# Optimization experiments

Hardware: AMD Instinct MI355X
Metric: run time of the kernel (lower is better)

Reference implementation:

```python
import jax, jax.numpy as jnp
import numpy as np

N = 50000   # nodes
E = 800000  # edges
H = 128     # hidden dim
V = 50000   # feats_per_node (embedding vocab)


def setup_inputs() -> dict:
    key = jax.random.key(0)
    ks = jax.random.split(key, 16)
    s = 0.05  # keep activations in a sane range
    return {
        "node_ids": jax.random.randint(ks[0], (N,), 0, V),
        "src": jax.random.randint(ks[1], (E,), 0, N),
        "dst": jnp.sort(jax.random.randint(ks[2], (E,), 0, N)),
        "emb": jax.random.normal(ks[3], (V, H), jnp.float32) * s,
        "W_pool1": jax.random.normal(ks[4], (H, H), jnp.float32) * s,
        "b_pool1": jax.random.normal(ks[5], (H,), jnp.float32) * s,
        "W_self1": jax.random.normal(ks[6], (H, H), jnp.float32) * s,
        "W_neigh1": jax.random.normal(ks[7], (H, H), jnp.float32) * s,
        "b1": jax.random.normal(ks[8], (H,), jnp.float32) * s,
        "W_pool2": jax.random.normal(ks[9], (H, H), jnp.float32) * s,
        "b_pool2": jax.random.normal(ks[10], (H,), jnp.float32) * s,
        "W_self2": jax.random.normal(ks[11], (H, H), jnp.float32) * s,
        "W_neigh2": jax.random.normal(ks[12], (H, H), jnp.float32) * s,
        "b2": jax.random.normal(ks[13], (H,), jnp.float32) * s,
    }


def _sage_pool_layer(h, src, dst, W_pool, b_pool, W_self, W_neigh, b):
    # DGL SAGEConv('pool'): per-src MLP, gather over edges, segmented max per dst.
    m = jax.nn.relu(h @ W_pool + b_pool)              # [N, H]
    msgs = m[src]                                     # [E, H] gather
    agg = jax.ops.segment_max(msgs, dst, num_segments=N,
                              indices_are_sorted=True)  # [N, H]
    agg = jnp.where(jnp.isneginf(agg), 0.0, agg)      # zero-in-degree -> 0 (DGL semantics)
    return h @ W_self + agg @ W_neigh + b


def reference(node_ids, src, dst, emb,
              W_pool1, b_pool1, W_self1, W_neigh1, b1,
              W_pool2, b_pool2, W_self2, W_neigh2, b2):
    h = emb[node_ids]                                 # embedding_h on 1-hot indices
    h = _sage_pool_layer(h, src, dst, W_pool1, b_pool1, W_self1, W_neigh1, b1)
    h = _sage_pool_layer(h, src, dst, W_pool2, b_pool2, W_self2, W_neigh2, b2)
    return h
```

## Files before the change

kernel.cpp:

```cpp
#include <hip/hip_runtime.h>

#define HD 128

typedef __attribute__((ext_vector_type(8))) short short8;
typedef __attribute__((ext_vector_type(4))) float floatx4;

typedef unsigned short ushort_t;
typedef unsigned int uint_t;

__device__ __forceinline__ ushort_t f2b(float f) {
    union { float f; uint_t u; } v; v.f = f;
    uint_t r = v.u + 0x7fff + ((v.u >> 16) & 1);
    return (ushort_t)(r >> 16);
}
__device__ __forceinline__ float b_lo(uint_t p) {
    union { uint_t u; float f; } v; v.u = p << 16; return v.f;
}
__device__ __forceinline__ float b_hi(uint_t p) {
    union { uint_t u; float f; } v; v.u = p & 0xffff0000u; return v.f;
}
__device__ __forceinline__ uint_t packb(float a, float b) {
    union { float f; uint_t u; } x, y; x.f = a; y.f = b;
    return (x.u >> 16) | (y.u & 0xffff0000u);
}
__device__ __forceinline__ short8 cvt8(const float* __restrict__ p) {
    float4 u = *(const float4*)p, v = *(const float4*)(p + 4);
    short8 r;
    r[0] = (short)f2b(u.x); r[1] = (short)f2b(u.y); r[2] = (short)f2b(u.z); r[3] = (short)f2b(u.w);
    r[4] = (short)f2b(v.x); r[5] = (short)f2b(v.y); r[6] = (short)f2b(v.z); r[7] = (short)f2b(v.w);
    return r;
}

__global__ __launch_bounds__(256) void k_prep(const int* __restrict__ dst, int E,
                                              int* __restrict__ rp, int N,
                                              const float* W0, const float* W1,
                                              const float* W2, const float* W3,
                                              const float* W4, const float* W5,
                                              ushort_t* __restrict__ Wpk, int nbR) {
    int b = blockIdx.x;
    if (b < nbR) {
        int i = b * 256 + threadIdx.x;
        if (i > N) return;
        int lo = 0, hi = E;
        while (lo < hi) {
            int mid = (lo + hi) >> 1;
            if (dst[mid] < i) lo = mid + 1; else hi = mid;
        }
        rp[i] = lo;
    } else {
        int bb = b - nbR;
        const float* Ws[6] = {W0, W1, W2, W3, W4, W5};
        int mat = bb >> 6;
        int o = ((bb & 63) << 8) + threadIdx.x;
        int j = o & 7, l = (o >> 3) & 63, s = (o >> 9) & 3, t = o >> 11;
        int k = s * 32 + ((l >> 4) & 3) * 8 + j;
        int n = t * 16 + (l & 15);
        Wpk[(size_t)mat * 16384 + o] = f2b(Ws[mat][k * HD + n]);
    }
}

__device__ __forceinline__ void stage_w(const ushort_t* __restrict__ g,
                                        ushort_t* l, int tid) {
#pragma unroll
    for (int i = 0; i < 8; ++i) {
        int off = i * 2048 + tid * 8;
        *(short8*)&l[off] = *(const short8*)&g[off];
    }
}

__device__ __forceinline__ void store_bf16(ushort_t* __restrict__ m, int row,
                                           int colbase, const floatx4& acc,
                                           const float4& bv, bool relu, int N) {
    if (row >= N) return;
    float v0 = acc[0] + bv.x, v1 = acc[1] + bv.y, v2 = acc[2] + bv.z, v3 = acc[3] + bv.w;
    if (relu) { v0 = fmaxf(v0, 0.f); v1 = fmaxf(v1, 0.f); v2 = fmaxf(v2, 0.f); v3 = fmaxf(v3, 0.f); }
    uint2 o; o.x = (uint_t)f2b(v0) | ((uint_t)f2b(v1) << 16);
    o.y = (uint_t)f2b(v2) | ((uint_t)f2b(v3) << 16);
    *(uint2*)&m[(size_t)row * HD + colbase] = o;
}

__global__ __launch_bounds__(256) void k_gather_pool(const int* __restrict__ ids,
                                                     const float* __restrict__ emb,
                                                     const ushort_t* __restrict__ Wpk,
                                                     const float* __restrict__ bias,
                                                     ushort_t* __restrict__ h0,
                                                     ushort_t* __restrict__ m, int N) {
    __shared__ ushort_t Wl[16384];
    int wave = blockIdx.x * 4 + (threadIdx.x >> 6);
    int row0 = wave * 32;
    int l = threadIdx.x & 63;
    int ar0 = row0 + (l & 15); if (ar0 >= N) ar0 = N - 1;
    int ar1 = ar0 + 16;        if (ar1 >= N) ar1 = N - 1;
    int ac = (l >> 4) * 8;
    int id0 = ids[ar0], id1 = ids[ar1];
    short8 a0[4], a1[4];
#pragma unroll
    for (int s = 0; s < 4; ++s) {
        a0[s] = cvt8(&emb[(size_t)id0 * HD + s * 32 + ac]);
        a1[s] = cvt8(&emb[(size_t)id1 * HD + s * 32 + ac]);
    }
    stage_w(Wpk, Wl, threadIdx.x);
    __syncthreads();
    if (row0 >= N) return;
#pragma unroll
    for (int s = 0; s < 4; ++s) {
        *(short8*)&h0[(size_t)ar0 * HD + s * 32 + ac] = a0[s];
        *(short8*)&h0[(size_t)ar1 * HD + s * 32 + ac] = a1[s];
    }
    int g0 = row0 + (l & 15), g1 = g0 + 16;
    int cb0 = ((l >> 4) & 3) * 4;
#pragma unroll
    for (int t = 0; t < 8; ++t) {
        floatx4 acc0 = {0.f, 0.f, 0.f, 0.f};
        floatx4 acc1 = {0.f, 0.f, 0.f, 0.f};
#pragma unroll
        for (int s = 0; s < 4; ++s) {
            short8 w = *(const short8*)&Wl[(t * 4 + s) * 512 + l * 8];
            acc0 = __builtin_amdgcn_mfma_f32_16x16x32_bf16(w, a0[s], acc0, 0, 0, 0);
            acc1 = __builtin_amdgcn_mfma_f32_16x16x32_bf16(w, a1[s], acc1, 0, 0, 0);
        }
        int cb = t * 16 + cb0;
        float4 bv = *(const float4*)&bias[cb];
        store_bf16(m, g0, cb, acc0, bv, true, N);
        store_bf16(m, g1, cb, acc1, bv, true, N);
    }
}

__global__ __launch_bounds__(256) void k_pool(const ushort_t* __restrict__ h,
                                              const ushort_t* __restrict__ Wpk,
                                              const float* __restrict__ bias,
                                              ushort_t* __restrict__ m, int N) {
    __shared__ ushort_t Wl[16384];
    int wave = blockIdx.x * 4 + (threadIdx.x >> 6);
    int row0 = wave * 32;
    int l = threadIdx.x & 63;
    int ar0 = row0 + (l & 15); if (ar0 >= N) ar0 = N - 1;
    int ar1 = ar0 + 16;        if (ar1 >= N) ar1 = N - 1;
    int ac = (l >> 4) * 8;
    short8 a0[4], a1[4];
#pragma unroll
    for (int s = 0; s < 4; ++s) {
        a0[s] = *(const short8*)&h[(size_t)ar0 * HD + s * 32 + ac];
        a1[s] = *(const short8*)&h[(size_t)ar1 * HD + s * 32 + ac];
    }
    stage_w(Wpk, Wl, threadIdx.x);
    __syncthreads();
    if (row0 >= N) return;
    int g0 = row0 + (l & 15), g1 = g0 + 16;
    int cb0 = ((l >> 4) & 3) * 4;
#pragma unroll
    for (int t = 0; t < 8; ++t) {
        floatx4 acc0 = {0.f, 0.f, 0.f, 0.f};
        floatx4 acc1 = {0.f, 0.f, 0.f, 0.f};
#pragma unroll
        for (int s = 0; s < 4; ++s) {
            short8 w = *(const short8*)&Wl[(t * 4 + s) * 512 + l * 8];
            acc0 = __builtin_amdgcn_mfma_f32_16x16x32_bf16(w, a0[s], acc0, 0, 0, 0);
            acc1 = __builtin_amdgcn_mfma_f32_16x16x32_bf16(w, a1[s], acc1, 0, 0, 0);
        }
        int cb = t * 16 + cb0;
        float4 bv = *(const float4*)&bias[cb];
        store_bf16(m, g0, cb, acc0, bv, true, N);
        store_bf16(m, g1, cb, acc1, bv, true, N);
    }
}

__global__ __launch_bounds__(256) void k_segmax(const ushort_t* __restrict__ m,
                                                const int* __restrict__ src,
                                                const int* __restrict__ rp,
                                                ushort_t* __restrict__ agg, int N) {
    int node = blockIdx.x * 4 + (threadIdx.x >> 6);
    if (node >= N) return;
    int l = threadIdx.x & 63;
    int slot = l >> 4;
    int col8 = (l & 15) * 8;
    int beg = rp[node], end = rp[node + 1];
    float a[8] = {0.f, 0.f, 0.f, 0.f, 0.f, 0.f, 0.f, 0.f};
    float c[8] = {0.f, 0.f, 0.f, 0.f, 0.f, 0.f, 0.f, 0.f};
    for (int base = beg; base < end; base += 64) {
        int nb = end - base; if (nb > 64) nb = 64;
        int si = base + l; if (si > end - 1) si = end - 1;
        int sv = src[si];
        for (int o = 0; o < nb; o += 16) {
            int last = nb - 1;
            int i0 = o + slot;      if (i0 > last) i0 = last;
            int i1 = o + 4 + slot;  if (i1 > last) i1 = last;
            int i2 = o + 8 + slot;  if (i2 > last) i2 = last;
            int i3 = o + 12 + slot; if (i3 > last) i3 = last;
            int s0 = __shfl(sv, i0), s1 = __shfl(sv, i1);
            int s2 = __shfl(sv, i2), s3 = __shfl(sv, i3);
            uint4 p0 = *(const uint4*)&m[(size_t)s0 * HD + col8];
            uint4 p1 = *(const uint4*)&m[(size_t)s1 * HD + col8];
            uint4 p2 = *(const uint4*)&m[(size_t)s2 * HD + col8];
            uint4 p3 = *(const uint4*)&m[(size_t)s3 * HD + col8];
            a[0] = fmaxf(a[0], b_lo(p0.x)); a[1] = fmaxf(a[1], b_hi(p0.x));
            a[2] = fmaxf(a[2], b_lo(p0.y)); a[3] = fmaxf(a[3], b_hi(p0.y));
            a[4] = fmaxf(a[4], b_lo(p0.z)); a[5] = fmaxf(a[5], b_hi(p0.z));
            a[6] = fmaxf(a[6], b_lo(p0.w)); a[7] = fmaxf(a[7], b_hi(p0.w));
            c[0] = fmaxf(c[0], b_lo(p1.x)); c[1] = fmaxf(c[1], b_hi(p1.x));
            c[2] = fmaxf(c[2], b_lo(p1.y)); c[3] = fmaxf(c[3], b_hi(p1.y));
            c[4] = fmaxf(c[4], b_lo(p1.z)); c[5] = fmaxf(c[5], b_hi(p1.z));
            c[6] = fmaxf(c[6], b_lo(p1.w)); c[7] = fmaxf(c[7], b_hi(p1.w));
            a[0] = fmaxf(a[0], b_lo(p2.x)); a[1] = fmaxf(a[1], b_hi(p2.x));
            a[2] = fmaxf(a[2], b_lo(p2.y)); a[3] = fmaxf(a[3], b_hi(p2.y));
            a[4] = fmaxf(a[4], b_lo(p2.z)); a[5] = fmaxf(a[5], b_hi(p2.z));
            a[6] = fmaxf(a[6], b_lo(p2.w)); a[7] = fmaxf(a[7], b_hi(p2.w));
            c[0] = fmaxf(c[0], b_lo(p3.x)); c[1] = fmaxf(c[1], b_hi(p3.x));
            c[2] = fmaxf(c[2], b_lo(p3.y)); c[3] = fmaxf(c[3], b_hi(p3.y));
            c[4] = fmaxf(c[4], b_lo(p3.z)); c[5] = fmaxf(c[5], b_hi(p3.z));
            c[6] = fmaxf(c[6], b_lo(p3.w)); c[7] = fmaxf(c[7], b_hi(p3.w));
        }
    }
#pragma unroll
    for (int i = 0; i < 8; ++i) {
        a[i] = fmaxf(a[i], c[i]);
        a[i] = fmaxf(a[i], __shfl_xor(a[i], 16));
        a[i] = fmaxf(a[i], __shfl_xor(a[i], 32));
    }
    if (slot == 0) {
        uint4 o;
        o.x = packb(a[0], a[1]); o.y = packb(a[2], a[3]);
        o.z = packb(a[4], a[5]); o.w = packb(a[6], a[7]);
        *(uint4*)&agg[(size_t)node * HD + col8] = o;
    }
}

template <bool F32OUT>
__global__ __launch_bounds__(256) void k_dual(const ushort_t* __restrict__ h,
                                              const ushort_t* __restrict__ agg,
                                              const ushort_t* __restrict__ WsPk,
                                              const ushort_t* __restrict__ WnPk,
                                              const float* __restrict__ bias,
                                              void* __restrict__ outp, int N) {
    __shared__ ushort_t Wl[32768];
    int wave = blockIdx.x * 4 + (threadIdx.x >> 6);
    int row0 = wave * 32;
    int l = threadIdx.x & 63;
    int ar0 = row0 + (l & 15); if (ar0 >= N) ar0 = N - 1;
    int ar1 = ar0 + 16;        if (ar1 >= N) ar1 = N - 1;
    int ac = (l >> 4) * 8;
    short8 ah0[4], ah1[4], ag0[4], ag1[4];
#pragma unroll
    for (int s = 0; s < 4; ++s) {
        ah0[s] = *(const short8*)&h[(size_t)ar0 * HD + s * 32 + ac];
        ah1[s] = *(const short8*)&h[(size_t)ar1 * HD + s * 32 + ac];
        ag0[s] = *(const short8*)&agg[(size_t)ar0 * HD + s * 32 + ac];
        ag1[s] = *(const short8*)&agg[(size_t)ar1 * HD + s * 32 + ac];
    }
    stage_w(WsPk, Wl, threadIdx.x);
    stage_w(WnPk, Wl + 16384, threadIdx.x);
    __syncthreads();
    if (row0 >= N) return;
    int g0 = row0 + (l & 15), g1 = g0 + 16;
    int cb0 = ((l >> 4) & 3) * 4;
#pragma unroll
    for (int t = 0; t < 8; ++t) {
        floatx4 acc0 = {0.f, 0.f, 0.f, 0.f};
        floatx4 acc1 = {0.f, 0.f, 0.f, 0.f};
#pragma unroll
        for (int s = 0; s < 4; ++s) {
            short8 ws = *(const short8*)&Wl[(t * 4 + s) * 512 + l * 8];
            acc0 = __builtin_amdgcn_mfma_f32_16x16x32_bf16(ws, ah0[s], acc0, 0, 0, 0);
            acc1 = __builtin_amdgcn_mfma_f32_16x16x32_bf16(ws, ah1[s], acc1, 0, 0, 0);
        }
#pragma unroll
        for (int s = 0; s < 4; ++s) {
            short8 wn = *(const short8*)&Wl[16384 + (t * 4 + s) * 512 + l * 8];
            acc0 = __builtin_amdgcn_mfma_f32_16x16x32_bf16(wn, ag0[s], acc0, 0, 0, 0);
            acc1 = __builtin_amdgcn_mfma_f32_16x16x32_bf16(wn, ag1[s], acc1, 0, 0, 0);
        }
        int cb = t * 16 + cb0;
        float4 bv = *(const float4*)&bias[cb];
        if (F32OUT) {
            float* out = (float*)outp;
            if (g0 < N) {
                float4 v = make_float4(acc0[0] + bv.x, acc0[1] + bv.y,
                                       acc0[2] + bv.z, acc0[3] + bv.w);
                *(float4*)&out[(size_t)g0 * HD + cb] = v;
            }
            if (g1 < N) {
                float4 v = make_float4(acc1[0] + bv.x, acc1[1] + bv.y,
                                       acc1[2] + bv.z, acc1[3] + bv.w);
                *(float4*)&out[(size_t)g1 * HD + cb] = v;
            }
        } else {
            ushort_t* out = (ushort_t*)outp;
            store_bf16(out, g0, cb, acc0, bv, false, N);
            store_bf16(out, g1, cb, acc1, bv, false, N);
        }
    }
}

extern "C" void kernel_launch(void* const* d_in, const int* in_sizes, int n_in,
                              void* d_out, int out_size, void* d_ws, size_t ws_size,
                              hipStream_t stream) {
    const int*   node_ids = (const int*)d_in[0];
    const int*   src      = (const int*)d_in[1];
    const int*   dst      = (const int*)d_in[2];
    const float* emb      = (const float*)d_in[3];
    const float* Wp1      = (const float*)d_in[4];
    const float* bp1      = (const float*)d_in[5];
    const float* Ws1      = (const float*)d_in[6];
    const float* Wn1      = (const float*)d_in[7];
    const float* b1       = (const float*)d_in[8];
    const float* Wp2      = (const float*)d_in[9];
    const float* bp2      = (const float*)d_in[10];
    const float* Ws2      = (const float*)d_in[11];
    const float* Wn2      = (const float*)d_in[12];
    const float* b2       = (const float*)d_in[13];
    float* out = (float*)d_out;

    const int N = in_sizes[0];
    const int E = in_sizes[1];

    char* ws = (char*)d_ws;
    int* rp = (int*)ws;
    size_t off = (((size_t)(N + 1) * 4) + 255) & ~(size_t)255;
    ushort_t* Wpk  = (ushort_t*)(ws + off);
    ushort_t* h0   = Wpk + 6 * 16384;
    ushort_t* h1   = h0 + (size_t)N * HD;
    ushort_t* bufM = h1 + (size_t)N * HD;
    ushort_t* bufA = bufM + (size_t)N * HD;

    const int nbR = (N + 1 + 255) / 256;
    const int nbP = 6 * 64;
    const int nb_gemm = (N + 127) / 128;
    const int nb_seg  = (N + 3) / 4;

    k_prep<<<nbR + nbP, 256, 0, stream>>>(dst, E, rp, N,
                                          Wp1, Ws1, Wn1, Wp2, Ws2, Wn2, Wpk, nbR);

    const ushort_t* Wp1k = Wpk;
    const ushort_t* Ws1k = Wpk + 16384;
    const ushort_t* Wn1k = Wpk + 2 * 16384;
    const ushort_t* Wp2k = Wpk + 3 * 16384;
    const ushort_t* Ws2k = Wpk + 4 * 16384;
    const ushort_t* Wn2k = Wpk + 5 * 16384;

    k_gather_pool<<<nb_gemm, 256, 0, stream>>>(node_ids, emb, Wp1k, bp1, h0, bufM, N);
    k_segmax<<<nb_seg, 256, 0, stream>>>(bufM, src, rp, bufA, N);
    k_dual<false><<<nb_gemm, 256, 0, stream>>>(h0, bufA, Ws1k, Wn1k, b1, h1, N);
    k_pool<<<nb_gemm, 256, 0, stream>>>(h1, Wp2k, bp2, bufM, N);
    k_segmax<<<nb_seg, 256, 0, stream>>>(bufM, src, rp, bufA, N);
    k_dual<true><<<nb_gemm, 256, 0, stream>>>(h1, bufA, Ws2k, Wn2k, b2, out, N);
}
```

Measured before the change: 214.4 us.

## Store pool messages column-blocked and segmax on packed bf16 per column group

The pool GEMM now writes its ReLU output in a column-blocked layout: eight slabs of 16 columns, each holding all N rows contiguously. The segment-max kernel is split so that each block works on one 16-column group, which keeps that slab's 1.6 MB footprint cache-resident during the random src gathers. Each lane does packed 2x bf16 integer max instead of unpacking to fp32. Unsigned-short max is only valid because ReLU makes every value non-negative, and each node's edges are now re-read once per column group, so the src index loads grow eightfold.

```diff
diff --git a/kernel.cpp b/kernel.cpp
--- a/kernel.cpp
+++ b/kernel.cpp
@@ -4,6 +4,7 @@
 
 typedef __attribute__((ext_vector_type(8))) short short8;
 typedef __attribute__((ext_vector_type(4))) float floatx4;
+typedef __attribute__((ext_vector_type(2))) unsigned short ushort2v;
 
 typedef unsigned short ushort_t;
 typedef unsigned int uint_t;
@@ -12,16 +13,6 @@
     union { float f; uint_t u; } v; v.f = f;
     uint_t r = v.u + 0x7fff + ((v.u >> 16) & 1);
     return (ushort_t)(r >> 16);
-}
-__device__ __forceinline__ float b_lo(uint_t p) {
-    union { uint_t u; float f; } v; v.u = p << 16; return v.f;
-}
-__device__ __forceinline__ float b_hi(uint_t p) {
-    union { uint_t u; float f; } v; v.u = p & 0xffff0000u; return v.f;
-}
-__device__ __forceinline__ uint_t packb(float a, float b) {
-    union { float f; uint_t u; } x, y; x.f = a; y.f = b;
-    return (x.u >> 16) | (y.u & 0xffff0000u);
 }
 __device__ __forceinline__ short8 cvt8(const float* __restrict__ p) {
     float4 u = *(const float4*)p, v = *(const float4*)(p + 4);
@@ -29,6 +20,11 @@
     r[0] = (short)f2b(u.x); r[1] = (short)f2b(u.y); r[2] = (short)f2b(u.z); r[3] = (short)f2b(u.w);
     r[4] = (short)f2b(v.x); r[5] = (short)f2b(v.y); r[6] = (short)f2b(v.z); r[7] = (short)f2b(v.w);
     return r;
+}
+__device__ __forceinline__ uint_t pkmax(uint_t a, uint_t b) {
+    return __builtin_bit_cast(uint_t,
+        __builtin_elementwise_max(__builtin_bit_cast(ushort2v, a),
+                                  __builtin_bit_cast(ushort2v, b)));
 }
 
 __global__ __launch_bounds__(256) void k_prep(const int* __restrict__ dst, int E,
@@ -77,6 +73,19 @@
     uint2 o; o.x = (uint_t)f2b(v0) | ((uint_t)f2b(v1) << 16);
     o.y = (uint_t)f2b(v2) | ((uint_t)f2b(v3) << 16);
     *(uint2*)&m[(size_t)row * HD + colbase] = o;
+}
+
+__device__ __forceinline__ void store_m(ushort_t* __restrict__ m, int row,
+                                        int colbase, const floatx4& acc,
+                                        const float4& bv, int N) {
+    if (row >= N) return;
+    float v0 = fmaxf(acc[0] + bv.x, 0.f), v1 = fmaxf(acc[1] + bv.y, 0.f);
+    float v2 = fmaxf(acc[2] + bv.z, 0.f), v3 = fmaxf(acc[3] + bv.w, 0.f);
+    uint2 o; o.x = (uint_t)f2b(v0) | ((uint_t)f2b(v1) << 16);
+    o.y = (uint_t)f2b(v2) | ((uint_t)f2b(v3) << 16);
+    size_t addr = (size_t)(colbase >> 4) * ((size_t)N * 16)
+                + (size_t)row * 16 + (colbase & 15);
+    *(uint2*)&m[addr] = o;
 }
 
 __global__ __launch_bounds__(256) void k_gather_pool(const int* __restrict__ ids,
@@ -121,8 +130,8 @@
         }
         int cb = t * 16 + cb0;
         float4 bv = *(const float4*)&bias[cb];
-        store_bf16(m, g0, cb, acc0, bv, true, N);
-        store_bf16(m, g1, cb, acc1, bv, true, N);
+        store_m(m, g0, cb, acc0, bv, N);
+        store_m(m, g1, cb, acc1, bv, N);
     }
 }
 
@@ -160,8 +169,8 @@
         }
         int cb = t * 16 + cb0;
         float4 bv = *(const float4*)&bias[cb];
-        store_bf16(m, g0, cb, acc0, bv, true, N);
-        store_bf16(m, g1, cb, acc1, bv, true, N);
+        store_m(m, g0, cb, acc0, bv, N);
+        store_m(m, g1, cb, acc1, bv, N);
     }
 }
 
@@ -169,59 +178,40 @@
                                                 const int* __restrict__ src,
                                                 const int* __restrict__ rp,
                                                 ushort_t* __restrict__ agg, int N) {
-    int node = blockIdx.x * 4 + (threadIdx.x >> 6);
-    if (node >= N) return;
+    int cg = blockIdx.x & 7;
     int l = threadIdx.x & 63;
-    int slot = l >> 4;
-    int col8 = (l & 15) * 8;
-    int beg = rp[node], end = rp[node + 1];
-    float a[8] = {0.f, 0.f, 0.f, 0.f, 0.f, 0.f, 0.f, 0.f};
-    float c[8] = {0.f, 0.f, 0.f, 0.f, 0.f, 0.f, 0.f, 0.f};
-    for (int base = beg; base < end; base += 64) {
-        int nb = end - base; if (nb > 64) nb = 64;
-        int si = base + l; if (si > end - 1) si = end - 1;
-        int sv = src[si];
-        for (int o = 0; o < nb; o += 16) {
-            int last = nb - 1;
-            int i0 = o + slot;      if (i0 > last) i0 = last;
-            int i1 = o + 4 + slot;  if (i1 > last) i1 = last;
-            int i2 = o + 8 + slot;  if (i2 > last) i2 = last;
-            int i3 = o + 12 + slot; if (i3 > last) i3 = last;
-            int s0 = __shfl(sv, i0), s1 = __shfl(sv, i1);
-            int s2 = __shfl(sv, i2), s3 = __shfl(sv, i3);
-            uint4 p0 = *(const uint4*)&m[(size_t)s0 * HD + col8];
-            uint4 p1 = *(const uint4*)&m[(size_t)s1 * HD + col8];
-            uint4 p2 = *(const uint4*)&m[(size_t)s2 * HD + col8];
-            uint4 p3 = *(const uint4*)&m[(size_t)s3 * HD + col8];
-            a[0] = fmaxf(a[0], b_lo(p0.x)); a[1] = fmaxf(a[1], b_hi(p0.x));
-            a[2] = fmaxf(a[2], b_lo(p0.y)); a[3] = fmaxf(a[3], b_hi(p0.y));
-            a[4] = fmaxf(a[4], b_lo(p0.z)); a[5] = fmaxf(a[5], b_hi(p0.z));
-            a[6] = fmaxf(a[6], b_lo(p0.w)); a[7] = fmaxf(a[7], b_hi(p0.w));
-            c[0] = fmaxf(c[0], b_lo(p1.x)); c[1] = fmaxf(c[1], b_hi(p1.x));
-            c[2] = fmaxf(c[2], b_lo(p1.y)); c[3] = fmaxf(c[3], b_hi(p1.y));
-            c[4] = fmaxf(c[4], b_lo(p1.z)); c[5] = fmaxf(c[5], b_hi(p1.z));
-            c[6] = fmaxf(c[6], b_lo(p1.w)); c[7] = fmaxf(c[7], b_hi(p1.w));
-            a[0] = fmaxf(a[0], b_lo(p2.x)); a[1] = fmaxf(a[1], b_hi(p2.x));
-            a[2] = fmaxf(a[2], b_lo(p2.y)); a[3] = fmaxf(a[3], b_hi(p2.y));
-            a[4] = fmaxf(a[4], b_lo(p2.z)); a[5] = fmaxf(a[5], b_hi(p2.z));
-            a[6] = fmaxf(a[6], b_lo(p2.w)); a[7] = fmaxf(a[7], b_hi(p2.w));
-            c[0] = fmaxf(c[0], b_lo(p3.x)); c[1] = fmaxf(c[1], b_hi(p3.x));
-            c[2] = fmaxf(c[2], b_lo(p3.y)); c[3] = fmaxf(c[3], b_hi(p3.y));
-            c[4] = fmaxf(c[4], b_lo(p3.z)); c[5] = fmaxf(c[5], b_hi(p3.z));
-            c[6] = fmaxf(c[6], b_lo(p3.w)); c[7] = fmaxf(c[7], b_hi(p3.w));
-        }
-    }
-#pragma unroll
-    for (int i = 0; i < 8; ++i) {
-        a[i] = fmaxf(a[i], c[i]);
-        a[i] = fmaxf(a[i], __shfl_xor(a[i], 16));
-        a[i] = fmaxf(a[i], __shfl_xor(a[i], 32));
-    }
-    if (slot == 0) {
-        uint4 o;
-        o.x = packb(a[0], a[1]); o.y = packb(a[2], a[3]);
-        o.z = packb(a[4], a[5]); o.w = packb(a[6], a[7]);
-        *(uint4*)&agg[(size_t)node * HD + col8] = o;
+    int slot = l >> 3;
+    int c = l & 7;
+    int node0 = ((blockIdx.x >> 3) * 4 + (threadIdx.x >> 6)) * 4;
+    const uint_t* __restrict__ mg = (const uint_t*)m + (size_t)cg * ((size_t)N * 8);
+    uint_t* __restrict__ aggw = (uint_t*)agg;
+#pragma unroll 1
+    for (int nn = 0; nn < 4; ++nn) {
+        int node = node0 + nn;
+        if (node >= N) return;
+        int beg = rp[node], end = rp[node + 1];
+        uint_t a = 0u, b = 0u;
+        for (int base = beg; base < end; base += 64) {
+            int nb = end - base; if (nb > 64) nb = 64;
+            int si = base + l; if (si > end - 1) si = end - 1;
+            int sv = __builtin_nontemporal_load(&src[si]);
+            for (int o = 0; o < nb; o += 16) {
+                int last = nb - 1;
+                int i0 = o + slot;     if (i0 > last) i0 = last;
+                int i1 = o + 8 + slot; if (i1 > last) i1 = last;
+                int s0 = __shfl(sv, i0), s1 = __shfl(sv, i1);
+                uint_t p0 = mg[(size_t)s0 * 8 + c];
+                uint_t p1 = mg[(size_t)s1 * 8 + c];
+                a = pkmax(a, p0);
+                b = pkmax(b, p1);
+            }
+        }
+        a = pkmax(a, b);
+        a = pkmax(a, (uint_t)__shfl_xor((int)a, 8));
+        a = pkmax(a, (uint_t)__shfl_xor((int)a, 16));
+        a = pkmax(a, (uint_t)__shfl_xor((int)a, 32));
+        if (slot == 0)
+            __builtin_nontemporal_store(a, &aggw[(size_t)node * 64 + cg * 8 + c]);
     }
 }
 
@@ -325,7 +315,7 @@
     const int nbR = (N + 1 + 255) / 256;
     const int nbP = 6 * 64;
     const int nb_gemm = (N + 127) / 128;
-    const int nb_seg  = (N + 3) / 4;
+    const int nb_seg  = ((N + 15) / 16) * 8;
 
     k_prep<<<nbR + nbP, 256, 0, stream>>>(dst, E, rp, N,
                                           Wp1, Ws1, Wn1, Wp2, Ws2, Wn2, Wpk, nbR);
```

After: 366.5 us. 1.71x slower.
